# Kernel tuning notes

Hardware: AMD Instinct MI355X
Metric: run time of the kernel (lower is better)

Reference implementation:

```python
import jax, jax.numpy as jnp
import numpy as np

EMBED_DIM = 1024
NB_HEADS = 16
HEAD_DIM = EMBED_DIM // NB_HEADS


def setup_inputs() -> dict:
    key = jax.random.key(0)
    ks = jax.random.split(key, 5)
    B, N, D = 4, 2048, EMBED_DIM
    scale = 1.0 / np.sqrt(D)
    return {
        "x": jax.random.normal(ks[0], (B, N, D), dtype=jnp.float32),
        "qkv_w": jax.random.normal(ks[1], (3 * D, D), dtype=jnp.float32) * scale,
        "qkv_b": jax.random.normal(ks[2], (3 * D,), dtype=jnp.float32) * 0.02,
        "proj_w": jax.random.normal(ks[3], (D, D), dtype=jnp.float32) * scale,
        "proj_b": jax.random.normal(ks[4], (D,), dtype=jnp.float32) * 0.02,
    }


def reference(x, qkv_w, qkv_b, proj_w, proj_b):
    B, N, D = x.shape
    H, Hd = NB_HEADS, HEAD_DIM
    # qkv projection: torch Linear => x @ W.T + b
    qkv = x @ qkv_w.T + qkv_b                       # [B, N, 3D]
    qkv = qkv.reshape(B, N, 3, H, Hd)
    q = jnp.transpose(qkv[:, :, 0], (0, 2, 1, 3))   # [B, H, N, Hd]
    k = jnp.transpose(qkv[:, :, 1], (0, 2, 1, 3))
    v = jnp.transpose(qkv[:, :, 2], (0, 2, 1, 3))
    scores = jnp.einsum("bhnd,bhmd->bhnm", q, k) * (Hd ** -0.5)  # [B,H,N,N]
    attn = jax.nn.softmax(scores, axis=-1)
    out = jnp.einsum("bhnm,bhmd->bhnd", attn, v)    # [B, H, N, Hd]
    out = jnp.transpose(out, (0, 2, 1, 3)).reshape(B, N, D)
    out = out @ proj_w.T + proj_b
    return out
```

## Files before the change

kernel.cpp:

```cpp
#include <hip/hip_runtime.h>


typedef __attribute__((ext_vector_type(8))) short bf16x8;
typedef __attribute__((ext_vector_type(4))) short s16x4;
typedef __attribute__((ext_vector_type(4))) float f32x4;
typedef __attribute__((ext_vector_type(16))) float f32x16;
typedef __attribute__((ext_vector_type(4))) unsigned u32x4;

#define LOG2E 1.44269504088896340736f

__device__ static inline short f2bf(float f) {
  unsigned u = __builtin_bit_cast(unsigned, f);
  unsigned r = (u + 0x7fffu + ((u >> 16) & 1u)) >> 16;
  return (short)r;
}
__device__ static inline unsigned cvtpk_bf16(float lo, float hi) {
  unsigned r;
  asm("v_cvt_pk_bf16_f32 %0, %1, %2" : "=v"(r) : "v"(lo), "v"(hi));
  return r;
}
__device__ static inline float exp2_hw(float x) {
#if __has_builtin(__builtin_amdgcn_exp2f)
  return __builtin_amdgcn_exp2f(x);
#else
  float r;
  asm("v_exp_f32 %0, %1" : "=v"(r) : "v"(x));
  return r;
#endif
}

__device__ static inline void gload_lds16(const void* g, void* l) {
  __builtin_amdgcn_global_load_lds(
      (const __attribute__((address_space(1))) void*)g,
      (__attribute__((address_space(3))) void*)l, 16, 0, 0);
}

__global__ void cvt_f32_bf16(const float* __restrict__ in, short* __restrict__ out, int n4) {
  int i = blockIdx.x * 256 + threadIdx.x;
  if (i < n4) {
    float4 v = ((const float4*)in)[i];
    s16x4 o4 = { f2bf(v.x), f2bf(v.y), f2bf(v.z), f2bf(v.w) };
    ((s16x4*)out)[i] = o4;
  }
}

__global__ __launch_bounds__(512, 2) void gemm_qkv(
    const short* __restrict__ A, const short* __restrict__ Bm,
    const float* __restrict__ bias,
    short* __restrict__ qo, short* __restrict__ ko, short* __restrict__ vto) {
  __shared__ __align__(16) char smem[131072];
  const int tid = threadIdx.x, lane = tid & 63, w = tid >> 6;
  const int wm = w >> 2, wn = w & 3;
  const int bn = blockIdx.x, bm = blockIdx.y;
  const int fr = lane & 15;
  const int cb0 = ((((lane >> 4))     ^ (lane & 7)) << 4);
  const int cb1 = ((((lane >> 4)) + 4 ^ (lane & 7)) << 4);

  char* ldsA0 = smem;
  char* ldsB0 = smem + 32768;
  char* ldsA1 = smem + 65536;
  char* ldsB1 = smem + 98304;

  const short* Ag = A + (size_t)(bm * 256) * 1024;
  const short* Bg = Bm + (size_t)(bn * 256) * 1024;

  auto STAGE = [&](const short* __restrict__ mg, int kt, int half, char* ldsmat) {
#pragma unroll
    for (int sw = 0; sw < 2; ++sw) {
      int r = half * 128 + sw * 64 + w * 8 + (lane >> 3);
      gload_lds16(mg + (size_t)r * 1024 + (kt & 15) * 64 + ((lane & 7) ^ (lane >> 3)) * 8,
                  ldsmat + (half * 128 + sw * 64 + w * 8) * 128);
    }
  };

  f32x4 acc[8][4];
  const f32x4 z4 = {0.f, 0.f, 0.f, 0.f};
#pragma unroll
  for (int i = 0; i < 8; ++i)
#pragma unroll
    for (int j = 0; j < 4; ++j) acc[i][j] = z4;

  bf16x8 a[4][2], b[2][2];

  STAGE(Ag, 0, 0, ldsA0);
  STAGE(Ag, 0, 1, ldsA0);
  STAGE(Bg, 0, 0, ldsB0);
  STAGE(Bg, 0, 1, ldsB0);
  STAGE(Ag, 1, 0, ldsA1);
  asm volatile("s_waitcnt vmcnt(2)" ::: "memory");
  __builtin_amdgcn_s_barrier();

#define PHASE(BUF, MH, NH, RDA, SG, SLDS, STILE, SHALF, W2)                    \
  {                                                                            \
    const char* Ab_ = smem + (BUF) * 65536;                                    \
    const char* Bb_ = Ab_ + 32768;                                             \
    if (RDA) {                                                                 \
      _Pragma("unroll")                                                        \
      for (int mf = 0; mf < 4; ++mf) {                                         \
        const char* ar = Ab_ + (wm * 128 + (MH) * 64 + mf * 16 + fr) * 128;    \
        a[mf][0] = *(const bf16x8*)(ar + cb0);                                 \
        a[mf][1] = *(const bf16x8*)(ar + cb1);                                 \
      }                                                                        \
    }                                                                          \
    _Pragma("unroll")                                                          \
    for (int nf = 0; nf < 2; ++nf) {                                           \
      const char* br = Bb_ + (wn * 64 + (NH) * 32 + nf * 16 + fr) * 128;       \
      b[nf][0] = *(const bf16x8*)(br + cb0);                                   \
      b[nf][1] = *(const bf16x8*)(br + cb1);                                   \
    }                                                                          \
    STAGE(SG, STILE, SHALF, SLDS);                                             \
    __builtin_amdgcn_s_barrier();                                              \
    __builtin_amdgcn_sched_barrier(0);                                         \
    __builtin_amdgcn_s_setprio(1);                                             \
    _Pragma("unroll")                                                          \
    for (int mf = 0; mf < 4; ++mf) {                                           \
      _Pragma("unroll")                                                        \
      for (int nf = 0; nf < 2; ++nf) {                                         \
        acc[(MH)*4 + mf][(NH)*2 + nf] = __builtin_amdgcn_mfma_f32_16x16x32_bf16( \
            a[mf][0], b[nf][0], acc[(MH)*4 + mf][(NH)*2 + nf], 0, 0, 0);       \
        acc[(MH)*4 + mf][(NH)*2 + nf] = __builtin_amdgcn_mfma_f32_16x16x32_bf16( \
            a[mf][1], b[nf][1], acc[(MH)*4 + mf][(NH)*2 + nf], 0, 0, 0);       \
      }                                                                        \
    }                                                                          \
    __builtin_amdgcn_s_setprio(0);                                             \
    if (W2) asm volatile("s_waitcnt vmcnt(2)" ::: "memory");                   \
    __builtin_amdgcn_s_barrier();                                              \
    __builtin_amdgcn_sched_barrier(0);                                         \
  }

  for (int j = 0; j < 8; ++j) {
    const int t0 = 2 * j;
    PHASE(0, 0, 0, true,  Ag, ldsA1, t0 + 1, 1, false);
    PHASE(0, 0, 1, false, Bg, ldsB1, t0 + 1, 0, false);
    PHASE(0, 1, 0, true,  Bg, ldsB1, t0 + 1, 1, false);
    PHASE(0, 1, 1, false, Ag, ldsA0, t0 + 2, 0, true);
    PHASE(1, 0, 0, true,  Ag, ldsA0, t0 + 2, 1, false);
    PHASE(1, 0, 1, false, Bg, ldsB0, t0 + 2, 0, false);
    PHASE(1, 1, 0, true,  Bg, ldsB0, t0 + 2, 1, false);
    PHASE(1, 1, 1, false, Ag, ldsA1, t0 + 3, 0, true);
  }
#undef PHASE

  asm volatile("s_waitcnt vmcnt(0)" ::: "memory");

  const int which = bn >> 2;
  const int head = (bn & 3) * 4 + wn;
  const int batch = bm >> 3;
  const size_t bh = (size_t)batch * 16 + head;
  const int rbase = (bm & 7) * 256 + wm * 128 + ((lane >> 4) << 2);
#pragma unroll
  for (int nf16 = 0; nf16 < 4; ++nf16) {
    const int dd = nf16 * 16 + fr;
    const float bv = bias[bn * 256 + wn * 64 + dd];
#pragma unroll
    for (int mf = 0; mf < 8; ++mf) {
      const int nr0 = rbase + mf * 16;
      if (which == 2) {
        int nper = (nr0 & ~12) | ((nr0 & 4) << 1) | ((nr0 & 8) >> 1);
        s16x4 pk;
#pragma unroll
        for (int r = 0; r < 4; ++r) pk[r] = f2bf(acc[mf][nf16][r] + bv);
        *(s16x4*)(vto + (bh * 64 + dd) * 2048 + nper) = pk;
      } else if (which == 0) {
        short* dst = qo + (bh * 2048 + nr0) * 64 + dd;
#pragma unroll
        for (int r = 0; r < 4; ++r)
          dst[(size_t)r * 64] = f2bf((acc[mf][nf16][r] + bv) * (0.125f * LOG2E));
      } else {
        short* dst = ko + (bh * 2048 + nr0) * 64 + dd;
#pragma unroll
        for (int r = 0; r < 4; ++r) dst[(size_t)r * 64] = f2bf(acc[mf][nf16][r] + bv);
      }
    }
  }
}

template <int EPI>
__global__ __launch_bounds__(256, 2) void gemm_bt(
    const short* __restrict__ A, const short* __restrict__ Bm,
    const float* __restrict__ bias, int K,
    float* __restrict__ outf) {
  __shared__ __align__(16) char smem[16384];
  char* As = smem;
  char* Bs = smem + 8192;
  const int tid = threadIdx.x, lane = tid & 63, w = tid >> 6;
  const int wm = w >> 1, wn = w & 1;
  const int bm = blockIdx.y, bn = blockIdx.x;

  f32x4 acc[4][4];
  const f32x4 z4 = {0.f, 0.f, 0.f, 0.f};
#pragma unroll
  for (int m = 0; m < 4; ++m)
#pragma unroll
    for (int n = 0; n < 4; ++n) acc[m][n] = z4;

  const short* Abase = A + (size_t)bm * 128 * K;
  const short* Bbase = Bm + (size_t)bn * 128 * K;

  for (int k0 = 0; k0 < K; k0 += 32) {
#pragma unroll
    for (int j = 0; j < 2; ++j) {
      int ia = w * 2 + j;
      int row = ia * 16 + (lane >> 2);
      int cl = (lane & 3) ^ (row & 3);
      gload_lds16(Abase + (size_t)row * K + k0 + cl * 8, As + ia * 1024);
      gload_lds16(Bbase + (size_t)row * K + k0 + cl * 8, Bs + ia * 1024);
    }
    __syncthreads();

    bf16x8 af[4], bf[4];
#pragma unroll
    for (int m = 0; m < 4; ++m) {
      int r = wm * 64 + m * 16 + (lane & 15);
      af[m] = *(const bf16x8*)(As + r * 64 + ((((lane >> 4)) ^ (r & 3)) << 4));
    }
#pragma unroll
    for (int n = 0; n < 4; ++n) {
      int r = wn * 64 + n * 16 + (lane & 15);
      bf[n] = *(const bf16x8*)(Bs + r * 64 + ((((lane >> 4)) ^ (r & 3)) << 4));
    }
#pragma unroll
    for (int m = 0; m < 4; ++m)
#pragma unroll
      for (int n = 0; n < 4; ++n)
        acc[m][n] = __builtin_amdgcn_mfma_f32_16x16x32_bf16(af[m], bf[n], acc[m][n], 0, 0, 0);
    __syncthreads();
  }

#pragma unroll
  for (int nf = 0; nf < 4; ++nf) {
    int gn = bn * 128 + wn * 64 + nf * 16 + (lane & 15);
    float bv = bias[gn];
#pragma unroll
    for (int m = 0; m < 4; ++m) {
      int gm0 = bm * 128 + wm * 64 + m * 16 + ((lane >> 4) << 2);
      float* dst = outf + (size_t)gm0 * 1024 + gn;
#pragma unroll
      for (int r = 0; r < 4; ++r) dst[(size_t)r * 1024] = acc[m][nf][r] + bv;
    }
  }
}

#define BUILD_PF2(d0, d1, sv)                                                  \
  {                                                                            \
    u32x4 w0_ = {cvtpk_bf16(sv[0], sv[1]), cvtpk_bf16(sv[2], sv[3]),           \
                 cvtpk_bf16(sv[4], sv[5]), cvtpk_bf16(sv[6], sv[7])};          \
    d0 = __builtin_bit_cast(bf16x8, w0_);                                      \
    u32x4 w1_ = {cvtpk_bf16(sv[8], sv[9]), cvtpk_bf16(sv[10], sv[11]),         \
                 cvtpk_bf16(sv[12], sv[13]), cvtpk_bf16(sv[14], sv[15])};      \
    d1 = __builtin_bit_cast(bf16x8, w1_);                                      \
  }

__global__ __launch_bounds__(256, 3) void attn_kernel(
    const short* __restrict__ q, const short* __restrict__ kk,
    const short* __restrict__ vt, short* __restrict__ ao) {
  __shared__ __align__(16) char smem[32768];
  const int tid = threadIdx.x, lane = tid & 63, w = tid >> 6;
  const int r31 = lane & 31, h = lane >> 5;
  const int id = blockIdx.x;
  const int xcd = id & 7, p = id >> 3;
  const int bh = xcd * 8 + (p >> 4);
  const int qblk = p & 15;
  const int q0 = qblk * 128 + w * 32;

  const short* qptr = q + ((size_t)bh * 2048 + q0 + r31) * 64 + h * 8;
  const short* kgl = kk + (size_t)bh * 2048 * 64;
  const short* vgl = vt + (size_t)bh * 64 * 2048;

  const int srow = w * 16 + (lane >> 3);
  const int scol = ((lane & 7) * 8) ^ ((lane >> 3) << 3);
  const int ldst = w * 2048;

  bf16x8 qf[4];
#pragma unroll
  for (int dk = 0; dk < 4; ++dk) qf[dk] = *(const bf16x8*)(qptr + dk * 16);

  f32x16 o0, o1;
#pragma unroll
  for (int e = 0; e < 16; ++e) { o0[e] = 0.f; o1[e] = 0.f; }
  float ls[4];
#pragma unroll
  for (int e = 0; e < 4; ++e) ls[e] = 0.f;

#pragma unroll
  for (int j = 0; j < 2; ++j) {
    gload_lds16(kgl + (size_t)(srow + j * 8) * 64 + scol, smem + ldst + j * 1024);
    gload_lds16(vgl + (size_t)(srow + j * 8) * 2048 + scol, smem + 8192 + ldst + j * 1024);
  }
  __syncthreads();

  int cur = 0;
  for (int t = 0; t < 2048; t += 64) {
    const char* Kb = smem + cur * 16384;
    const char* Vb = smem + cur * 16384 + 8192;

    if (t + 64 < 2048) {
      char* nb = (char*)smem + (cur ^ 1) * 16384;
#pragma unroll
      for (int j = 0; j < 2; ++j) {
        gload_lds16(kgl + (size_t)(t + 64 + srow + j * 8) * 64 + scol, nb + ldst + j * 1024);
        gload_lds16(vgl + (size_t)(srow + j * 8) * 2048 + (t + 64) + scol, nb + 8192 + ldst + j * 1024);
      }
    }

    bf16x8 kf0[4], kf1[4];
#pragma unroll
    for (int dk = 0; dk < 4; ++dk) {
      int cb = (dk * 32 + h * 16) ^ ((r31 & 7) << 4);
      kf0[dk] = *(const bf16x8*)(Kb + r31 * 128 + cb);
      kf1[dk] = *(const bf16x8*)(Kb + (32 + r31) * 128 + cb);
    }

    f32x16 s0, s1;
#pragma unroll
    for (int e = 0; e < 16; ++e) { s0[e] = 0.f; s1[e] = 0.f; }
#pragma unroll
    for (int dk = 0; dk < 4; ++dk) {
      s0 = __builtin_amdgcn_mfma_f32_32x32x16_bf16(kf0[dk], qf[dk], s0, 0, 0, 0);
      s1 = __builtin_amdgcn_mfma_f32_32x32x16_bf16(kf1[dk], qf[dk], s1, 0, 0, 0);
    }

#pragma unroll
    for (int e = 0; e < 16; ++e) {
      s0[e] = exp2_hw(s0[e]);
      s1[e] = exp2_hw(s1[e]);
    }
#pragma unroll
    for (int e = 0; e < 4; ++e) {
      float t0 = (s0[e] + s0[e + 4]) + (s0[e + 8] + s0[e + 12]);
      float t1 = (s1[e] + s1[e + 4]) + (s1[e + 8] + s1[e + 12]);
      ls[e] += t0 + t1;
    }

    bf16x8 pf0, pf1, pf2, pf3;
    BUILD_PF2(pf0, pf1, s0);
    BUILD_PF2(pf2, pf3, s1);

    {
      bf16x8 v00, v10, v01, v11;
      int cb0 = (0 * 32 + h * 16) ^ ((r31 & 7) << 4);
      int cb1 = (1 * 32 + h * 16) ^ ((r31 & 7) << 4);
      v00 = *(const bf16x8*)(Vb + r31 * 128 + cb0);
      v10 = *(const bf16x8*)(Vb + (32 + r31) * 128 + cb0);
      v01 = *(const bf16x8*)(Vb + r31 * 128 + cb1);
      v11 = *(const bf16x8*)(Vb + (32 + r31) * 128 + cb1);
      o0 = __builtin_amdgcn_mfma_f32_32x32x16_bf16(v00, pf0, o0, 0, 0, 0);
      o1 = __builtin_amdgcn_mfma_f32_32x32x16_bf16(v10, pf0, o1, 0, 0, 0);
      o0 = __builtin_amdgcn_mfma_f32_32x32x16_bf16(v01, pf1, o0, 0, 0, 0);
      o1 = __builtin_amdgcn_mfma_f32_32x32x16_bf16(v11, pf1, o1, 0, 0, 0);
    }
    {
      bf16x8 v02, v12, v03, v13;
      int cb2 = (2 * 32 + h * 16) ^ ((r31 & 7) << 4);
      int cb3 = (3 * 32 + h * 16) ^ ((r31 & 7) << 4);
      v02 = *(const bf16x8*)(Vb + r31 * 128 + cb2);
      v12 = *(const bf16x8*)(Vb + (32 + r31) * 128 + cb2);
      v03 = *(const bf16x8*)(Vb + r31 * 128 + cb3);
      v13 = *(const bf16x8*)(Vb + (32 + r31) * 128 + cb3);
      o0 = __builtin_amdgcn_mfma_f32_32x32x16_bf16(v02, pf2, o0, 0, 0, 0);
      o1 = __builtin_amdgcn_mfma_f32_32x32x16_bf16(v12, pf2, o1, 0, 0, 0);
      o0 = __builtin_amdgcn_mfma_f32_32x32x16_bf16(v03, pf3, o0, 0, 0, 0);
      o1 = __builtin_amdgcn_mfma_f32_32x32x16_bf16(v13, pf3, o1, 0, 0, 0);
    }

    __syncthreads();
    cur ^= 1;
  }

  float lsum = (ls[0] + ls[1]) + (ls[2] + ls[3]);
  lsum += __shfl_xor(lsum, 32);

  const int b = bh >> 4, hd = bh & 15;
  float inv = 1.f / lsum;
  short* orow = ao + ((size_t)b * 2048 + q0 + r31) * 1024 + hd * 64;
#pragma unroll
  for (int s2 = 0; s2 < 4; ++s2) {
    s16x4 pk0, pk1;
#pragma unroll
    for (int r = 0; r < 4; ++r) {
      pk0[r] = f2bf(o0[4 * s2 + r] * inv);
      pk1[r] = f2bf(o1[4 * s2 + r] * inv);
    }
    *(s16x4*)(orow + 8 * s2 + 4 * h) = pk0;
    *(s16x4*)(orow + 32 + 8 * s2 + 4 * h) = pk1;
  }
}

extern "C" void kernel_launch(void* const* d_in, const int* in_sizes, int n_in,
                              void* d_out, int out_size, void* d_ws, size_t ws_size,
                              hipStream_t stream) {
  const float* x = (const float*)d_in[0];
  const float* qkv_w = (const float*)d_in[1];
  const float* qkv_b = (const float*)d_in[2];
  const float* proj_w = (const float*)d_in[3];
  const float* proj_b = (const float*)d_in[4];
  float* out = (float*)d_out;

  char* ws = (char*)d_ws;
  short* xb    = (short*)(ws + 0);
  short* wqkv  = (short*)(ws + 16777216);
  short* wproj = (short*)(ws + 23068672);
  short* qb    = (short*)(ws + 25165824);
  short* kb    = (short*)(ws + 41943040);
  short* vtb   = (short*)(ws + 58720256);
  short* aob   = (short*)(ws + 75497472);

  cvt_f32_bf16<<<8192, 256, 0, stream>>>(x, xb, 2097152);
  cvt_f32_bf16<<<3072, 256, 0, stream>>>(qkv_w, wqkv, 786432);
  cvt_f32_bf16<<<1024, 256, 0, stream>>>(proj_w, wproj, 262144);

  gemm_qkv<<<dim3(12, 32), 512, 0, stream>>>(xb, wqkv, qkv_b, qb, kb, vtb);
  attn_kernel<<<1024, 256, 0, stream>>>(qb, kb, vtb, aob);
  gemm_bt<1><<<dim3(8, 64), 256, 0, stream>>>(aob, wproj, proj_b, 1024, out);
}
```

Baseline: 199.3 us.

## Deepen QKV GEMM prefetch pipeline and remap blocks for L2 locality

The QKV GEMM now stages LDS tiles along the MFMA consumption order: A halves by m-half and B halves by n-half. Prefetches are issued earlier, and the vmcnt waits are relaxed from 2 to 8 outstanding loads, so more global loads stay in flight behind the MFMA phases. The grid is also flattened to 1D with a swizzled block-to-tile mapping, so that blocks likely to run together (consecutive IDs mod 8) share B weight tiles and nearby A rows, improving cache reuse. The relaxed waits depend on the exact phase ordering being correct; a mismatch would read stale LDS.

Result: no change. 201.9 us (+1.3%).

```diff
diff --git a/kernel.cpp b/kernel.cpp
--- a/kernel.cpp
+++ b/kernel.cpp
@@ -51,10 +51,13 @@
   __shared__ __align__(16) char smem[131072];
   const int tid = threadIdx.x, lane = tid & 63, w = tid >> 6;
   const int wm = w >> 2, wn = w & 3;
-  const int bn = blockIdx.x, bm = blockIdx.y;
+  const int id = blockIdx.x;
+  const int s = id >> 3;
+  const int bm = (id & 7) * 4 + (s & 3);
+  const int bn = s >> 2;
   const int fr = lane & 15;
-  const int cb0 = ((((lane >> 4))     ^ (lane & 7)) << 4);
-  const int cb1 = ((((lane >> 4)) + 4 ^ (lane & 7)) << 4);
+  const int cb0 = ((((lane >> 4))       ^ (lane & 7)) << 4);
+  const int cb1 = (((((lane >> 4)) + 4) ^ (lane & 7)) << 4);
 
   char* ldsA0 = smem;
   char* ldsB0 = smem + 32768;
@@ -64,12 +67,24 @@
   const short* Ag = A + (size_t)(bm * 256) * 1024;
   const short* Bg = Bm + (size_t)(bn * 256) * 1024;
 
-  auto STAGE = [&](const short* __restrict__ mg, int kt, int half, char* ldsmat) {
+  auto STAGE_A = [&](const short* __restrict__ mg, int kt, int h, char* lds) {
 #pragma unroll
     for (int sw = 0; sw < 2; ++sw) {
-      int r = half * 128 + sw * 64 + w * 8 + (lane >> 3);
-      gload_lds16(mg + (size_t)r * 1024 + (kt & 15) * 64 + ((lane & 7) ^ (lane >> 3)) * 8,
-                  ldsmat + (half * 128 + sw * 64 + w * 8) * 128);
+      int seg = w * 2 + sw;
+      int base = (seg < 8) ? (h * 64 + seg * 8) : (128 + h * 64 + (seg - 8) * 8);
+      gload_lds16(mg + (size_t)(base + (lane >> 3)) * 1024 + (kt & 15) * 64 +
+                      ((lane & 7) ^ (lane >> 3)) * 8,
+                  lds + base * 128);
+    }
+  };
+  auto STAGE_B = [&](const short* __restrict__ mg, int kt, int h, char* lds) {
+#pragma unroll
+    for (int sw = 0; sw < 2; ++sw) {
+      int seg = w * 2 + sw;
+      int base = (seg >> 2) * 64 + h * 32 + (seg & 3) * 8;
+      gload_lds16(mg + (size_t)(base + (lane >> 3)) * 1024 + (kt & 15) * 64 +
+                      ((lane & 7) ^ (lane >> 3)) * 8,
+                  lds + base * 128);
     }
   };
 
@@ -78,19 +93,21 @@
 #pragma unroll
   for (int i = 0; i < 8; ++i)
 #pragma unroll
-    for (int j = 0; j < 4; ++j) acc[i][j] = z4;
+    for (int jj = 0; jj < 4; ++jj) acc[i][jj] = z4;
 
   bf16x8 a[4][2], b[2][2];
 
-  STAGE(Ag, 0, 0, ldsA0);
-  STAGE(Ag, 0, 1, ldsA0);
-  STAGE(Bg, 0, 0, ldsB0);
-  STAGE(Bg, 0, 1, ldsB0);
-  STAGE(Ag, 1, 0, ldsA1);
-  asm volatile("s_waitcnt vmcnt(2)" ::: "memory");
+  STAGE_A(Ag, 0, 0, ldsA0);
+  STAGE_B(Bg, 0, 0, ldsB0);
+  STAGE_B(Bg, 0, 1, ldsB0);
+  STAGE_A(Ag, 0, 1, ldsA0);
+  STAGE_A(Ag, 1, 0, ldsA1);
+  STAGE_B(Bg, 1, 0, ldsB1);
+  STAGE_A(Ag, 1, 1, ldsA1);
+  asm volatile("s_waitcnt vmcnt(6)" ::: "memory");
   __builtin_amdgcn_s_barrier();
 
-#define PHASE(BUF, MH, NH, RDA, SG, SLDS, STILE, SHALF, W2)                    \
+#define PHASE(BUF, MH, NH, RDA, WAIT, ...)                                     \
   {                                                                            \
     const char* Ab_ = smem + (BUF) * 65536;                                    \
     const char* Bb_ = Ab_ + 32768;                                             \
@@ -108,7 +125,7 @@
       b[nf][0] = *(const bf16x8*)(br + cb0);                                   \
       b[nf][1] = *(const bf16x8*)(br + cb1);                                   \
     }                                                                          \
-    STAGE(SG, STILE, SHALF, SLDS);                                             \
+    __VA_ARGS__;                                                               \
     __builtin_amdgcn_s_barrier();                                              \
     __builtin_amdgcn_sched_barrier(0);                                         \
     __builtin_amdgcn_s_setprio(1);                                             \
@@ -123,21 +140,21 @@
       }                                                                        \
     }                                                                          \
     __builtin_amdgcn_s_setprio(0);                                             \
-    if (W2) asm volatile("s_waitcnt vmcnt(2)" ::: "memory");                   \
+    if (WAIT) asm volatile("s_waitcnt vmcnt(8)" ::: "memory");                 \
     __builtin_amdgcn_s_barrier();                                              \
     __builtin_amdgcn_sched_barrier(0);                                         \
   }
 
   for (int j = 0; j < 8; ++j) {
-    const int t0 = 2 * j;
-    PHASE(0, 0, 0, true,  Ag, ldsA1, t0 + 1, 1, false);
-    PHASE(0, 0, 1, false, Bg, ldsB1, t0 + 1, 0, false);
-    PHASE(0, 1, 0, true,  Bg, ldsB1, t0 + 1, 1, false);
-    PHASE(0, 1, 1, false, Ag, ldsA0, t0 + 2, 0, true);
-    PHASE(1, 0, 0, true,  Ag, ldsA0, t0 + 2, 1, false);
-    PHASE(1, 0, 1, false, Bg, ldsB0, t0 + 2, 0, false);
-    PHASE(1, 1, 0, true,  Bg, ldsB0, t0 + 2, 1, false);
-    PHASE(1, 1, 1, false, Ag, ldsA1, t0 + 3, 0, true);
+    const int t = 2 * j;
+    PHASE(0, 0, 0, true,  true,  STAGE_B(Bg, t + 1, 1, ldsB1));
+    PHASE(0, 0, 1, false, false, STAGE_A(Ag, t + 2, 0, ldsA0));
+    PHASE(0, 1, 0, true,  false, (void)0);
+    PHASE(0, 1, 1, false, true,  STAGE_A(Ag, t + 2, 1, ldsA0); STAGE_B(Bg, t + 2, 0, ldsB0));
+    PHASE(1, 0, 0, true,  true,  STAGE_B(Bg, t + 2, 1, ldsB0));
+    PHASE(1, 0, 1, false, false, STAGE_A(Ag, t + 3, 0, ldsA1));
+    PHASE(1, 1, 0, true,  false, (void)0);
+    PHASE(1, 1, 1, false, true,  STAGE_A(Ag, t + 3, 1, ldsA1); STAGE_B(Bg, t + 3, 0, ldsB1));
   }
 #undef PHASE
 
@@ -409,7 +426,7 @@
   cvt_f32_bf16<<<3072, 256, 0, stream>>>(qkv_w, wqkv, 786432);
   cvt_f32_bf16<<<1024, 256, 0, stream>>>(proj_w, wproj, 262144);
 
-  gemm_qkv<<<dim3(12, 32), 512, 0, stream>>>(xb, wqkv, qkv_b, qb, kb, vtb);
+  gemm_qkv<<<384, 512, 0, stream>>>(xb, wqkv, qkv_b, qb, kb, vtb);
   attn_kernel<<<1024, 256, 0, stream>>>(qb, kb, vtb, aob);
   gemm_bt<1><<<dim3(8, 64), 256, 0, stream>>>(aob, wproj, proj_b, 1024, out);
 }
```
